# Performance work log

Hardware: AMD Instinct MI355X
Metric: run time of the kernel (lower is better)

## Reference

```python
import jax, jax.numpy as jnp
import numpy as np

N_NODES = 50000
N_EDGES = 800000
N_GRAPHS = 64
EPS = 1e-5
NEG_SLOPE = 0.2


def gat_conv(x, src, dst, W, a_src, a_dst, bias, heads, ch):
    # x: [N, Fin]; W: [Fin, heads*ch]; a_src/a_dst: [heads, ch]; bias: [heads*ch]
    N = x.shape[0]
    h = (x @ W).reshape(N, heads, ch)                       # [N,H,C]
    s_src = jnp.sum(h * a_src, axis=-1)                     # [N,H]
    s_dst = jnp.sum(h * a_dst, axis=-1)                     # [N,H]
    scores = jax.nn.leaky_relu(s_src[src] + s_dst[dst], NEG_SLOPE)  # [E,H]
    m = jax.ops.segment_max(scores, dst, num_segments=N)    # segment softmax (stable)
    e = jnp.exp(scores - m[dst])
    denom = jax.ops.segment_sum(e, dst, num_segments=N)
    alpha = e / denom[dst]                                  # [E,H]
    msg = h[src] * alpha[:, :, None]                        # [E,H,C]
    out = jax.ops.segment_sum(msg, dst, num_segments=N)     # [N,H,C]
    return out.reshape(N, heads * ch) + bias


def batch_norm(x, gamma, beta):
    mu = jnp.mean(x, axis=0)
    var = jnp.var(x, axis=0)  # biased, as in torch BN forward (training mode)
    return gamma * (x - mu) * jax.lax.rsqrt(var + EPS) + beta


def setup_inputs() -> dict:
    key = jax.random.key(0)
    ks = jax.random.split(key, 20)
    x = jax.random.normal(ks[0], (N_NODES, 8), dtype=jnp.float32)
    edge_index = jax.random.randint(ks[1], (2, N_EDGES), 0, N_NODES, dtype=jnp.int32)
    batch = jnp.sort(jax.random.randint(ks[2], (N_NODES,), 0, N_GRAPHS, dtype=jnp.int32))
    g = lambda k, shape: jax.random.normal(k, shape, dtype=jnp.float32) * 0.1
    return {
        "x": x, "edge_index": edge_index, "batch": batch,
        "W1": g(ks[3], (8, 128)), "a_src1": g(ks[4], (4, 32)), "a_dst1": g(ks[5], (4, 32)),
        "b1": jnp.zeros((128,), jnp.float32), "g1": jnp.ones((128,), jnp.float32),
        "beta1": jnp.zeros((128,), jnp.float32),
        "W2": g(ks[6], (128, 256)), "a_src2": g(ks[7], (4, 64)), "a_dst2": g(ks[8], (4, 64)),
        "b2": jnp.zeros((256,), jnp.float32), "g2": jnp.ones((256,), jnp.float32),
        "beta2": jnp.zeros((256,), jnp.float32),
        "fc1_w": g(ks[9], (256, 128)), "fc1_b": jnp.zeros((128,), jnp.float32),
        "fc2_w": g(ks[10], (128, 64)), "fc2_b": jnp.zeros((64,), jnp.float32),
        "fc3_w": g(ks[11], (64, 1)), "fc3_b": jnp.zeros((1,), jnp.float32),
    }


def reference(x, edge_index, batch, W1, a_src1, a_dst1, b1, g1, beta1,
              W2, a_src2, a_dst2, b2, g2, beta2,
              fc1_w, fc1_b, fc2_w, fc2_b, fc3_w, fc3_b):
    N = x.shape[0]
    loop = jnp.arange(N, dtype=edge_index.dtype)
    src = jnp.concatenate([edge_index[0], loop])  # PyG GATConv adds self-loops
    dst = jnp.concatenate([edge_index[1], loop])

    h = gat_conv(x, src, dst, W1, a_src1, a_dst1, b1, heads=4, ch=32)
    h = jax.nn.elu(batch_norm(h, g1, beta1))
    h = gat_conv(h, src, dst, W2, a_src2, a_dst2, b2, heads=4, ch=64)
    h = jax.nn.elu(batch_norm(h, g2, beta2))

    # global mean pool over graphs
    sums = jax.ops.segment_sum(h, batch, num_segments=N_GRAPHS)
    counts = jax.ops.segment_sum(jnp.ones((N,), h.dtype), batch, num_segments=N_GRAPHS)
    pooled = sums / jnp.maximum(counts, 1.0)[:, None]       # [G,256]

    z = jax.nn.relu(pooled @ fc1_w + fc1_b)
    emb = jax.nn.relu(z @ fc2_w + fc2_b)
    out = emb @ fc3_w + fc3_b
    return out.reshape(-1)
```

## Files before the change

### kernel.cpp

```cpp
#include <hip/hip_runtime.h>
#include <hip/hip_bf16.h>
#include <cmath>

#define NSLOPE 0.2f
#define BN_EPS 1e-5f
#define DEGCAP 128

static __device__ __forceinline__ float lrelu(float v) { return v > 0.f ? v : NSLOPE * v; }

static __device__ __forceinline__ float wmax64(float v) {
#pragma unroll
  for (int off = 32; off; off >>= 1) v = fmaxf(v, __shfl_xor(v, off));
  return v;
}
static __device__ __forceinline__ float wsum64(float v) {
#pragma unroll
  for (int off = 32; off; off >>= 1) v += __shfl_xor(v, off);
  return v;
}
static __device__ __forceinline__ float rlf(float v, int j) {
  return __int_as_float(__builtin_amdgcn_readlane(__float_as_int(v), j));
}
static __device__ __forceinline__ unsigned short f2bf(float x) {
  __hip_bfloat16 h = __float2bfloat16(x);
  union { __hip_bfloat16 h; unsigned short u; } c; c.h = h; return c.u;
}
static __device__ __forceinline__ unsigned pack_bf16(float x, float y) {
  return (unsigned)f2bf(x) | ((unsigned)f2bf(y) << 16);
}
static __device__ __forceinline__ float bflo(unsigned p) { return __uint_as_float(p << 16); }
static __device__ __forceinline__ float bfhi(unsigned p) { return __uint_as_float(p & 0xffff0000u); }

__global__ void k_init(int* __restrict__ cnt, int N,
                       const float* __restrict__ W1, const float* __restrict__ as1,
                       const float* __restrict__ ad1, const float* __restrict__ W2,
                       const float* __restrict__ as2, const float* __restrict__ ad2,
                       float* __restrict__ q1s, float* __restrict__ q1d,
                       float* __restrict__ q2s, float* __restrict__ q2d) {
  int i = blockIdx.x * blockDim.x + threadIdx.x;
  int stride = gridDim.x * blockDim.x;
  for (int j = i; j < N; j += stride) cnt[j] = 0;
  if (blockIdx.x == 0) {
    int t = threadIdx.x;
    if (t < 32) {
      int k = t >> 2, h = t & 3;
      float s = 0.f, d = 0.f;
      for (int c = 0; c < 32; ++c) {
        float w = W1[k * 128 + h * 32 + c];
        s = fmaf(w, as1[h * 32 + c], s);
        d = fmaf(w, ad1[h * 32 + c], d);
      }
      q1s[t] = s; q1d[t] = d;
    }
    for (int idx = t; idx < 512; idx += 256) {
      int k = idx >> 2, h = idx & 3;
      float s = 0.f, d = 0.f;
      for (int c = 0; c < 64; ++c) {
        float w = W2[k * 256 + h * 64 + c];
        s = fmaf(w, as2[h * 64 + c], s);
        d = fmaf(w, ad2[h * 64 + c], d);
      }
      q2s[idx] = s; q2d[idx] = d;
    }
  }
}

__global__ void k_scatter(const int* __restrict__ esrc, const int* __restrict__ edst,
                          const int* __restrict__ batch, int E, int N,
                          int* __restrict__ cnt, int* __restrict__ srcs,
                          int* __restrict__ gstart) {
  int i = blockIdx.x * blockDim.x + threadIdx.x;
  int stride = gridDim.x * blockDim.x;
  int total = E + N;
  for (int j = i; j < total; j += stride) {
    int s, d;
    if (j < E) {
      s = esrc[j]; d = edst[j];
    } else {
      int n = j - E;
      s = n; d = n;
      int b = batch[n];
      if (n == 0) {
        for (int g = 0; g <= b; ++g) gstart[g] = 0;
      } else {
        int pb = batch[n - 1];
        if (pb != b)
          for (int g = pb + 1; g <= b; ++g) gstart[g] = n;
      }
      if (n == N - 1)
        for (int g = b + 1; g <= 64; ++g) gstart[g] = N;
    }
    int pos = atomicAdd(&cnt[d], 1);
    if (pos < DEGCAP) srcs[(size_t)d * DEGCAP + pos] = s;
  }
}

__global__ __launch_bounds__(256) void k_s1(const float* __restrict__ x,
                                            const float* __restrict__ q1s,
                                            const float* __restrict__ q1d,
                                            float* __restrict__ ssrc, float* __restrict__ sdst,
                                            int N) {
  __shared__ float qs[32], qd[32];
  int t = threadIdx.x;
  if (t < 32) { qs[t] = q1s[t]; qd[t] = q1d[t]; }
  __syncthreads();
  for (int n = blockIdx.x * 256 + t; n < N; n += gridDim.x * 256) {
    float4 x0 = *(const float4*)&x[n * 8];
    float4 x1 = *(const float4*)&x[n * 8 + 4];
    float xs[8] = {x0.x, x0.y, x0.z, x0.w, x1.x, x1.y, x1.z, x1.w};
    float4 rs = make_float4(0.f, 0.f, 0.f, 0.f);
    float4 rd = make_float4(0.f, 0.f, 0.f, 0.f);
#pragma unroll
    for (int k = 0; k < 8; ++k) {
      rs.x = fmaf(xs[k], qs[k * 4 + 0], rs.x);
      rs.y = fmaf(xs[k], qs[k * 4 + 1], rs.y);
      rs.z = fmaf(xs[k], qs[k * 4 + 2], rs.z);
      rs.w = fmaf(xs[k], qs[k * 4 + 3], rs.w);
      rd.x = fmaf(xs[k], qd[k * 4 + 0], rd.x);
      rd.y = fmaf(xs[k], qd[k * 4 + 1], rd.y);
      rd.z = fmaf(xs[k], qd[k * 4 + 2], rd.z);
      rd.w = fmaf(xs[k], qd[k * 4 + 3], rd.w);
    }
    *(float4*)&ssrc[n * 4] = rs;
    *(float4*)&sdst[n * 4] = rd;
  }
}

__global__ __launch_bounds__(64) void k_agg1(const float* __restrict__ x,
                                             const float* __restrict__ ssrc,
                                             const float* __restrict__ sdst,
                                             const int* __restrict__ cnt,
                                             const int* __restrict__ srcs,
                                             float* __restrict__ agg , int N) {
  int n = blockIdx.x * 64 + threadIdx.x;
  if (n >= N) return;
  int beg = n * DEGCAP;
  int end = beg + min(cnt[n], DEGCAP);
  float4 sd = *(const float4*)&sdst[n * 4];
  float m0 = -INFINITY, m1 = -INFINITY, m2 = -INFINITY, m3 = -INFINITY;
  for (int e = beg; e < end; ++e) {
    int s = srcs[e];
    float4 sv = *(const float4*)&ssrc[s * 4];
    m0 = fmaxf(m0, lrelu(sv.x + sd.x));
    m1 = fmaxf(m1, lrelu(sv.y + sd.y));
    m2 = fmaxf(m2, lrelu(sv.z + sd.z));
    m3 = fmaxf(m3, lrelu(sv.w + sd.w));
  }
  float d0 = 0.f, d1 = 0.f, d2 = 0.f, d3 = 0.f;
  float acc[4][8];
#pragma unroll
  for (int h = 0; h < 4; ++h)
#pragma unroll
    for (int k = 0; k < 8; ++k) acc[h][k] = 0.f;
  const float4* x4 = (const float4*)x;
  for (int e = beg; e < end; ++e) {
    int s = srcs[e];
    float4 sv = *(const float4*)&ssrc[s * 4];
    float w0 = expf(lrelu(sv.x + sd.x) - m0);
    float w1 = expf(lrelu(sv.y + sd.y) - m1);
    float w2 = expf(lrelu(sv.z + sd.z) - m2);
    float w3 = expf(lrelu(sv.w + sd.w) - m3);
    d0 += w0; d1 += w1; d2 += w2; d3 += w3;
    float4 xa = x4[(size_t)s * 2];
    float4 xb = x4[(size_t)s * 2 + 1];
    float xs[8] = {xa.x, xa.y, xa.z, xa.w, xb.x, xb.y, xb.z, xb.w};
    float ws[4] = {w0, w1, w2, w3};
#pragma unroll
    for (int h = 0; h < 4; ++h)
#pragma unroll
      for (int k = 0; k < 8; ++k) acc[h][k] = fmaf(ws[h], xs[k], acc[h][k]);
  }
  float dd[4] = {d0, d1, d2, d3};
#pragma unroll
  for (int h = 0; h < 4; ++h) {
    float inv = 1.0f / dd[h];
    float4 oA = make_float4(acc[h][0] * inv, acc[h][1] * inv, acc[h][2] * inv, acc[h][3] * inv);
    float4 oB = make_float4(acc[h][4] * inv, acc[h][5] * inv, acc[h][6] * inv, acc[h][7] * inv);
    *(float4*)&agg[n * 32 + h * 8] = oA;
    *(float4*)&agg[n * 32 + h * 8 + 4] = oB;
  }
}

__global__ __launch_bounds__(128) void k_stats1(const float* __restrict__ agg,
                                                const float* __restrict__ W1,
                                                const float* __restrict__ b1,
                                                float* __restrict__ part, int N) {
  int t = threadIdx.x;
  __shared__ float ag[32];
  float bb = b1[t];
  float wc[8];
#pragma unroll
  for (int k = 0; k < 8; ++k) wc[k] = W1[k * 128 + t];
  int h = t >> 5;
  float s = 0.f, s2 = 0.f;
  for (int n = blockIdx.x; n < N; n += gridDim.x) {
    if (t < 32) ag[t] = agg[n * 32 + t];
    __syncthreads();
    float v = bb;
#pragma unroll
    for (int k = 0; k < 8; ++k) v = fmaf(ag[h * 8 + k], wc[k], v);
    s += v; s2 += v * v;
    __syncthreads();
  }
  part[(size_t)blockIdx.x * 256 + t] = s;
  part[(size_t)blockIdx.x * 256 + 128 + t] = s2;
}

template <int NB, int TWO_F>
__global__ __launch_bounds__(256) void k_bnreduce2(const float* __restrict__ part,
                                                   float* __restrict__ stat) {
  int j = blockIdx.x, t = threadIdx.x;
  float s = 0.f;
  for (int b = t; b < NB; b += 256) s += part[(size_t)b * TWO_F + j];
#pragma unroll
  for (int off = 32; off; off >>= 1) s += __shfl_xor(s, off);
  __shared__ float red[4];
  if ((t & 63) == 0) red[t >> 6] = s;
  __syncthreads();
  if (t == 0) stat[j] = (red[0] + red[1]) + (red[2] + red[3]);
}

__global__ __launch_bounds__(256) void k_bns2(const float* __restrict__ agg,
                                              const float* __restrict__ W1,
                                              const float* __restrict__ b1,
                                              unsigned* __restrict__ a1h_u,
                                              const float* __restrict__ sum,
                                              const float* __restrict__ sq,
                                              const float* __restrict__ gamma,
                                              const float* __restrict__ beta,
                                              const float* __restrict__ q2s,
                                              const float* __restrict__ q2d,
                                              float* __restrict__ ssrc2,
                                              float* __restrict__ sdst2, int N) {
  int w = threadIdx.x >> 6, l = threadIdx.x & 63;
  int n = blockIdx.x * 4 + w;
  if (n >= N) return;
  int c0 = 2 * l, c1 = 2 * l + 1;
  int h = l >> 4;
  float ag[8];
#pragma unroll
  for (int k = 0; k < 8; ++k) ag[k] = agg[n * 32 + h * 8 + k];
  float v0 = b1[c0], v1 = b1[c1];
#pragma unroll
  for (int k = 0; k < 8; ++k) {
    v0 = fmaf(ag[k], W1[k * 128 + c0], v0);
    v1 = fmaf(ag[k], W1[k * 128 + c1], v1);
  }
  float invN = 1.0f / N;
  float mean0 = sum[c0] * invN, mean1 = sum[c1] * invN;
  float var0 = sq[c0] * invN - mean0 * mean0;
  float var1 = sq[c1] * invN - mean1 * mean1;
  float iv0 = rsqrtf(var0 + BN_EPS), iv1 = rsqrtf(var1 + BN_EPS);
  float y0 = gamma[c0] * ((v0 - mean0) * iv0) + beta[c0];
  float y1 = gamma[c1] * ((v1 - mean1) * iv1) + beta[c1];
  y0 = y0 > 0.f ? y0 : expm1f(y0);
  y1 = y1 > 0.f ? y1 : expm1f(y1);
  a1h_u[(size_t)n * 64 + l] = pack_bf16(y0, y1);
  float4 qs0 = *(const float4*)&q2s[c0 * 4];
  float4 qs1 = *(const float4*)&q2s[c1 * 4];
  float4 qd0 = *(const float4*)&q2d[c0 * 4];
  float4 qd1 = *(const float4*)&q2d[c1 * 4];
  float p0 = fmaf(y1, qs1.x, y0 * qs0.x);
  float p1 = fmaf(y1, qs1.y, y0 * qs0.y);
  float p2 = fmaf(y1, qs1.z, y0 * qs0.z);
  float p3 = fmaf(y1, qs1.w, y0 * qs0.w);
  float d0 = fmaf(y1, qd1.x, y0 * qd0.x);
  float d1 = fmaf(y1, qd1.y, y0 * qd0.y);
  float d2 = fmaf(y1, qd1.z, y0 * qd0.z);
  float d3 = fmaf(y1, qd1.w, y0 * qd0.w);
#pragma unroll
  for (int off = 32; off; off >>= 1) {
    p0 += __shfl_xor(p0, off); p1 += __shfl_xor(p1, off);
    p2 += __shfl_xor(p2, off); p3 += __shfl_xor(p3, off);
    d0 += __shfl_xor(d0, off); d1 += __shfl_xor(d1, off);
    d2 += __shfl_xor(d2, off); d3 += __shfl_xor(d3, off);
  }
  if (l == 0) {
    *(float4*)&ssrc2[n * 4] = make_float4(p0, p1, p2, p3);
    *(float4*)&sdst2[n * 4] = make_float4(d0, d1, d2, d3);
  }
}

__global__ __launch_bounds__(256) void k_agg2(const unsigned short* __restrict__ a1h,
                                              const float* __restrict__ ssrc,
                                              const float* __restrict__ sdst,
                                              const int* __restrict__ cnt,
                                              const int* __restrict__ srcs,
                                              unsigned* __restrict__ aggh , int N) {
  int wid = threadIdx.x >> 6, l = threadIdx.x & 63;
  int n = blockIdx.x * 4 + wid;
  if (n >= N) return;
  int beg = n * DEGCAP;
  int deg = min(cnt[n], DEGCAP);
  float4 sd = *(const float4*)&sdst[n * 4];
  float m0 = -INFINITY, m1 = -INFINITY, m2 = -INFINITY, m3 = -INFINITY;
  float d0 = 0.f, d1 = 0.f, d2 = 0.f, d3 = 0.f;
  float2 ac0 = {0.f, 0.f}, ac1 = {0.f, 0.f}, ac2 = {0.f, 0.f}, ac3 = {0.f, 0.f};
  for (int c0 = 0; c0 < deg; c0 += 64) {
    int e = c0 + l;
    bool act = e < deg;
    int s = act ? srcs[beg + e] : 0;
    float4 sv = *(const float4*)&ssrc[s * 4];
    float v0 = act ? lrelu(sv.x + sd.x) : -INFINITY;
    float v1 = act ? lrelu(sv.y + sd.y) : -INFINITY;
    float v2 = act ? lrelu(sv.z + sd.z) : -INFINITY;
    float v3 = act ? lrelu(sv.w + sd.w) : -INFINITY;
    float nm0 = fmaxf(m0, wmax64(v0)), nm1 = fmaxf(m1, wmax64(v1));
    float nm2 = fmaxf(m2, wmax64(v2)), nm3 = fmaxf(m3, wmax64(v3));
    float sc0 = expf(m0 - nm0), sc1 = expf(m1 - nm1);
    float sc2 = expf(m2 - nm2), sc3 = expf(m3 - nm3);
    m0 = nm0; m1 = nm1; m2 = nm2; m3 = nm3;
    float ev0 = act ? expf(v0 - m0) : 0.f;
    float ev1 = act ? expf(v1 - m1) : 0.f;
    float ev2 = act ? expf(v2 - m2) : 0.f;
    float ev3 = act ? expf(v3 - m3) : 0.f;
    d0 = d0 * sc0 + wsum64(ev0);
    d1 = d1 * sc1 + wsum64(ev1);
    d2 = d2 * sc2 + wsum64(ev2);
    d3 = d3 * sc3 + wsum64(ev3);
    ac0.x *= sc0; ac0.y *= sc0; ac1.x *= sc1; ac1.y *= sc1;
    ac2.x *= sc2; ac2.y *= sc2; ac3.x *= sc3; ac3.y *= sc3;
    int cn = min(64, deg - c0);
    int cn4 = (cn + 3) & ~3;
    for (int j = 0; j < cn4; j += 4) {
      int sA = __builtin_amdgcn_readlane(s, j);
      int sB = __builtin_amdgcn_readlane(s, j + 1);
      int sC = __builtin_amdgcn_readlane(s, j + 2);
      int sD = __builtin_amdgcn_readlane(s, j + 3);
      unsigned pA = *(const unsigned*)&a1h[(size_t)sA * 128 + 2 * l];
      unsigned pB = *(const unsigned*)&a1h[(size_t)sB * 128 + 2 * l];
      unsigned pC = *(const unsigned*)&a1h[(size_t)sC * 128 + 2 * l];
      unsigned pD = *(const unsigned*)&a1h[(size_t)sD * 128 + 2 * l];
      float wA0 = rlf(ev0, j),     wA1 = rlf(ev1, j),     wA2 = rlf(ev2, j),     wA3 = rlf(ev3, j);
      float wB0 = rlf(ev0, j + 1), wB1 = rlf(ev1, j + 1), wB2 = rlf(ev2, j + 1), wB3 = rlf(ev3, j + 1);
      float wC0 = rlf(ev0, j + 2), wC1 = rlf(ev1, j + 2), wC2 = rlf(ev2, j + 2), wC3 = rlf(ev3, j + 2);
      float wD0 = rlf(ev0, j + 3), wD1 = rlf(ev1, j + 3), wD2 = rlf(ev2, j + 3), wD3 = rlf(ev3, j + 3);
      float ax, ay;
      ax = bflo(pA); ay = bfhi(pA);
      ac0.x = fmaf(wA0, ax, ac0.x); ac0.y = fmaf(wA0, ay, ac0.y);
      ac1.x = fmaf(wA1, ax, ac1.x); ac1.y = fmaf(wA1, ay, ac1.y);
      ac2.x = fmaf(wA2, ax, ac2.x); ac2.y = fmaf(wA2, ay, ac2.y);
      ac3.x = fmaf(wA3, ax, ac3.x); ac3.y = fmaf(wA3, ay, ac3.y);
      ax = bflo(pB); ay = bfhi(pB);
      ac0.x = fmaf(wB0, ax, ac0.x); ac0.y = fmaf(wB0, ay, ac0.y);
      ac1.x = fmaf(wB1, ax, ac1.x); ac1.y = fmaf(wB1, ay, ac1.y);
      ac2.x = fmaf(wB2, ax, ac2.x); ac2.y = fmaf(wB2, ay, ac2.y);
      ac3.x = fmaf(wB3, ax, ac3.x); ac3.y = fmaf(wB3, ay, ac3.y);
      ax = bflo(pC); ay = bfhi(pC);
      ac0.x = fmaf(wC0, ax, ac0.x); ac0.y = fmaf(wC0, ay, ac0.y);
      ac1.x = fmaf(wC1, ax, ac1.x); ac1.y = fmaf(wC1, ay, ac1.y);
      ac2.x = fmaf(wC2, ax, ac2.x); ac2.y = fmaf(wC2, ay, ac2.y);
      ac3.x = fmaf(wC3, ax, ac3.x); ac3.y = fmaf(wC3, ay, ac3.y);
      ax = bflo(pD); ay = bfhi(pD);
      ac0.x = fmaf(wD0, ax, ac0.x); ac0.y = fmaf(wD0, ay, ac0.y);
      ac1.x = fmaf(wD1, ax, ac1.x); ac1.y = fmaf(wD1, ay, ac1.y);
      ac2.x = fmaf(wD2, ax, ac2.x); ac2.y = fmaf(wD2, ay, ac2.y);
      ac3.x = fmaf(wD3, ax, ac3.x); ac3.y = fmaf(wD3, ay, ac3.y);
    }
  }
  size_t pl = (size_t)N * 64;
  size_t base = (size_t)n * 64 + l;
  float i0 = 1.0f / d0, i1 = 1.0f / d1, i2 = 1.0f / d2, i3 = 1.0f / d3;
  aggh[base] = pack_bf16(ac0.x * i0, ac0.y * i0);
  aggh[pl + base] = pack_bf16(ac1.x * i1, ac1.y * i1);
  aggh[2 * pl + base] = pack_bf16(ac2.x * i2, ac2.y * i2);
  aggh[3 * pl + base] = pack_bf16(ac3.x * i3, ac3.y * i3);
}

__global__ __launch_bounds__(256) void k_post2(const unsigned short* __restrict__ aggh,
                                               const float* __restrict__ W2,
                                               const float* __restrict__ b2,
                                               unsigned* __restrict__ o2h,
                                               float* __restrict__ part, int N) {
  __shared__ float As[64][64];
  __shared__ float Bs[64][64];
  int h = blockIdx.y;
  int m0 = blockIdx.x * 64;
  int tid = threadIdx.x;
  const unsigned short* Ap = aggh + (size_t)h * N * 128;
  int tx = tid & 15, ty = tid >> 4;
  float acc[4][4];
#pragma unroll
  for (int r = 0; r < 4; ++r)
#pragma unroll
    for (int c = 0; c < 4; ++c) acc[r][c] = 0.f;

#pragma unroll
  for (int kc = 0; kc < 2; ++kc) {
    {
      int ml = tid & 63, kg = tid >> 6;
      const unsigned short* arow = Ap + (size_t)(m0 + ml) * 128 + kc * 64 + kg * 16;
      bool rok = (m0 + ml) < N;
#pragma unroll
      for (int it = 0; it < 2; ++it) {
        uint4 q = rok ? *(const uint4*)(arow + it * 8) : make_uint4(0, 0, 0, 0);
        int kb = kg * 16 + it * 8;
        As[kb + 0][ml] = bflo(q.x); As[kb + 1][ml] = bfhi(q.x);
        As[kb + 2][ml] = bflo(q.y); As[kb + 3][ml] = bfhi(q.y);
        As[kb + 4][ml] = bflo(q.z); As[kb + 5][ml] = bfhi(q.z);
        As[kb + 6][ml] = bflo(q.w); As[kb + 7][ml] = bfhi(q.w);
      }
    }
    {
      int c4 = tid & 15, k0 = tid >> 4;
      for (int k = k0; k < 64; k += 16) {
        float4 v = *(const float4*)&W2[(size_t)(kc * 64 + k) * 256 + h * 64 + c4 * 4];
        *(float4*)&Bs[k][c4 * 4] = v;
      }
    }
    __syncthreads();
#pragma unroll 2
    for (int k = 0; k < 64; ++k) {
      float4 a4 = *(const float4*)&As[k][ty * 4];
      float4 b4 = *(const float4*)&Bs[k][tx * 4];
      float av[4] = {a4.x, a4.y, a4.z, a4.w};
      float bv[4] = {b4.x, b4.y, b4.z, b4.w};
#pragma unroll
      for (int r = 0; r < 4; ++r)
#pragma unroll
        for (int c = 0; c < 4; ++c) acc[r][c] = fmaf(av[r], bv[c], acc[r][c]);
    }
    __syncthreads();
  }

  float4 bb = *(const float4*)&b2[h * 64 + tx * 4];
  float ps[4] = {0.f, 0.f, 0.f, 0.f};
  float pq[4] = {0.f, 0.f, 0.f, 0.f};
#pragma unroll
  for (int r = 0; r < 4; ++r) {
    int row = m0 + ty * 4 + r;
    if (row < N) {
      float4 c4;
      c4.x = acc[r][0] + bb.x; c4.y = acc[r][1] + bb.y;
      c4.z = acc[r][2] + bb.z; c4.w = acc[r][3] + bb.w;
      uint2 pw;
      pw.x = pack_bf16(c4.x, c4.y);
      pw.y = pack_bf16(c4.z, c4.w);
      *(uint2*)&o2h[(size_t)row * 128 + (h * 64 + tx * 4) / 2] = pw;
      ps[0] += c4.x; pq[0] += c4.x * c4.x;
      ps[1] += c4.y; pq[1] += c4.y * c4.y;
      ps[2] += c4.z; pq[2] += c4.z * c4.z;
      ps[3] += c4.w; pq[3] += c4.w * c4.w;
    }
  }
  __syncthreads();
  float* red = &As[0][0];
#pragma unroll
  for (int c = 0; c < 4; ++c) {
    red[ty * 64 + tx * 4 + c] = ps[c];
    red[1024 + ty * 64 + tx * 4 + c] = pq[c];
  }
  __syncthreads();
  if (tid < 128) {
    int isq = tid >> 6, col = tid & 63;
    float s = 0.f;
#pragma unroll
    for (int w = 0; w < 16; ++w) s += red[isq * 1024 + w * 64 + col];
    part[((size_t)blockIdx.x * 4 + h) * 128 + isq * 64 + col] = s;
  }
}

__global__ __launch_bounds__(256) void k_bnredpost(const float* __restrict__ part, int nmb,
                                                   float* __restrict__ stat) {
  int j = blockIdx.x;
  int isq = j >> 8, col = j & 255;
  int h = col >> 6, cw = col & 63;
  int t = threadIdx.x;
  float s = 0.f;
  for (int mb = t; mb < nmb; mb += 256) s += part[((size_t)mb * 4 + h) * 128 + isq * 64 + cw];
#pragma unroll
  for (int off = 32; off; off >>= 1) s += __shfl_xor(s, off);
  __shared__ float red[4];
  if ((t & 63) == 0) red[t >> 6] = s;
  __syncthreads();
  if (t == 0) stat[j] = (red[0] + red[1]) + (red[2] + red[3]);
}

__global__ __launch_bounds__(256) void k_poolbn(const unsigned* __restrict__ o2h,
                                                const int* __restrict__ gstart,
                                                const float* __restrict__ sum,
                                                const float* __restrict__ sq,
                                                const float* __restrict__ gamma,
                                                const float* __restrict__ beta,
                                                float* __restrict__ part, int N) {
  int g = blockIdx.x, by = blockIdx.y, t = threadIdx.x;
  float mean = sum[t] * (1.0f / N);
  float var = sq[t] * (1.0f / N) - mean * mean;
  float inv = rsqrtf(var + BN_EPS);
  float ga = gamma[t], be = beta[t];
  int r0 = gstart[g], r1 = gstart[g + 1];
  int u = t >> 1, hi = t & 1;
  float s = 0.f;
  for (int base = r0 + by * 128; base < r1; base += 16 * 128) {
    int lim = min(r1, base + 128);
    for (int r = base; r < lim; ++r) {
      unsigned pw = o2h[(size_t)r * 128 + u];
      float v = hi ? bfhi(pw) : bflo(pw);
      float y = ga * ((v - mean) * inv) + be;
      s += (y > 0.f ? y : expm1f(y));
    }
  }
  part[((size_t)g * 16 + by) * 256 + t] = s;
}

__global__ __launch_bounds__(256) void k_head(const float* __restrict__ poolpart,
                                              const int* __restrict__ gstart,
                                              const float* __restrict__ w1, const float* __restrict__ b1,
                                              const float* __restrict__ w2, const float* __restrict__ b2,
                                              const float* __restrict__ w3, const float* __restrict__ b3,
                                              float* __restrict__ out) {
  __shared__ float p[256], z1[128], z2[64];
  int g = blockIdx.x, t = threadIdx.x;
  float s0 = 0.f;
#pragma unroll
  for (int b = 0; b < 16; ++b) s0 += poolpart[((size_t)g * 16 + b) * 256 + t];
  float cnt = (float)(gstart[g + 1] - gstart[g]);
  p[t] = s0 / fmaxf(cnt, 1.0f);
  __syncthreads();
  if (t < 128) {
    float s = b1[t];
    for (int k = 0; k < 256; ++k) s = fmaf(p[k], w1[k * 128 + t], s);
    z1[t] = fmaxf(s, 0.f);
  }
  __syncthreads();
  if (t < 64) {
    float s = b2[t];
    for (int k = 0; k < 128; ++k) s = fmaf(z1[k], w2[k * 64 + t], s);
    z2[t] = fmaxf(s, 0.f);
  }
  __syncthreads();
  if (t < 64) {
    float s = z2[t] * w3[t];
#pragma unroll
    for (int off = 32; off; off >>= 1) s += __shfl_xor(s, off);
    if (t == 0) out[g] = s + b3[0];
  }
}

extern "C" void kernel_launch(void* const* d_in, const int* in_sizes, int n_in,
                              void* d_out, int out_size, void* d_ws, size_t ws_size,
                              hipStream_t stream) {
  const float* x    = (const float*)d_in[0];
  const int*   eidx = (const int*)d_in[1];
  const int*   batch= (const int*)d_in[2];
  const float* W1   = (const float*)d_in[3];
  const float* as1  = (const float*)d_in[4];
  const float* ad1  = (const float*)d_in[5];
  const float* b1   = (const float*)d_in[6];
  const float* g1   = (const float*)d_in[7];
  const float* be1  = (const float*)d_in[8];
  const float* W2   = (const float*)d_in[9];
  const float* as2  = (const float*)d_in[10];
  const float* ad2  = (const float*)d_in[11];
  const float* b2   = (const float*)d_in[12];
  const float* g2   = (const float*)d_in[13];
  const float* be2  = (const float*)d_in[14];
  const float* fc1w = (const float*)d_in[15];
  const float* fc1b = (const float*)d_in[16];
  const float* fc2w = (const float*)d_in[17];
  const float* fc2b = (const float*)d_in[18];
  const float* fc3w = (const float*)d_in[19];
  const float* fc3b = (const float*)d_in[20];
  float* out = (float*)d_out;
  (void)n_in; (void)out_size; (void)ws_size;

  int N = in_sizes[0] / 8;
  int E = in_sizes[1] / 2;
  const int* esrc = eidx;
  const int* edst = eidx + E;
  int nmb = (N + 63) / 64;

  char* w = (char*)d_ws;
  auto take = [&](size_t bytes) -> char* {
    char* r = w;
    w += (bytes + 255) & ~(size_t)255;
    return r;
  };
  int*   cnt     = (int*)take(4 * (size_t)N);
  int*   srcs    = (int*)take(4 * (size_t)N * DEGCAP);
  int*   gstart  = (int*)take(4 * 65);
  float* bnstat  = (float*)take(4 * 1024);
  float* bnpart  = (float*)take(4 * 524288);
  float* pp2     = (float*)take(4 * (size_t)nmb * 512);
  float* poolpart= (float*)take(4 * 64 * 16 * 256);
  float* q1s     = (float*)take(4 * 32);
  float* q1d     = (float*)take(4 * 32);
  float* q2s     = (float*)take(4 * 512);
  float* q2d     = (float*)take(4 * 512);
  float* ssrc1   = (float*)take(16 * (size_t)N);
  float* sdst1   = (float*)take(16 * (size_t)N);
  float* ssrc2   = (float*)take(16 * (size_t)N);
  float* sdst2   = (float*)take(16 * (size_t)N);
  float* agg1    = (float*)take(4 * (size_t)N * 32);
  unsigned short* a1h  = (unsigned short*)take(2 * (size_t)N * 128);
  unsigned short* aggh = (unsigned short*)take(2 * (size_t)N * 512);
  unsigned* o2h  = (unsigned*)take(4 * (size_t)N * 128);

  float* sum1 = bnstat;       float* sq1 = bnstat + 128;
  float* sum2 = bnstat + 256; float* sq2 = bnstat + 512;

  k_init<<<196, 256, 0, stream>>>(cnt, N, W1, as1, ad1, W2, as2, ad2, q1s, q1d, q2s, q2d);
  k_scatter<<<2048, 256, 0, stream>>>(esrc, edst, batch, E, N, cnt, srcs, gstart);

  k_s1<<<256, 256, 0, stream>>>(x, q1s, q1d, ssrc1, sdst1, N);
  k_agg1<<<(N + 63) / 64, 64, 0, stream>>>(x, ssrc1, sdst1, cnt, srcs, agg1, N);
  k_stats1<<<2048, 128, 0, stream>>>(agg1, W1, b1, bnpart, N);
  k_bnreduce2<2048, 256><<<256, 256, 0, stream>>>(bnpart, bnstat);
  k_bns2<<<(N + 3) / 4, 256, 0, stream>>>(agg1, W1, b1, (unsigned*)a1h, sum1, sq1, g1, be1,
                                          q2s, q2d, ssrc2, sdst2, N);

  k_agg2<<<(N + 3) / 4, 256, 0, stream>>>(a1h, ssrc2, sdst2, cnt, srcs, (unsigned*)aggh, N);
  k_post2<<<dim3(nmb, 4), 256, 0, stream>>>(aggh, W2, b2, o2h, pp2, N);
  k_bnredpost<<<512, 256, 0, stream>>>(pp2, nmb, sum2);

  k_poolbn<<<dim3(64, 16), 256, 0, stream>>>(o2h, gstart, sum2, sq2, g2, be2, poolpart, N);
  k_head<<<64, 256, 0, stream>>>(poolpart, gstart, fc1w, fc1b, fc2w, fc2b, fc3w, fc3b, out);
}
```

Before: 335.3 us.

## Split agg1 per head, stage agg2 weights in LDS, merge init into scatter

k_agg1 now uses four threads per node, one per head, instead of one thread per node. This spreads the gather and FMA work across more lanes and cuts per-thread register use. k_agg2 writes the per-chunk softmax weights and source indices to shared memory and reads them back as vectors, replacing many readlane instructions. The separate init kernel is replaced by a memset, and the attention-vector precompute is folded into the scatter kernel, removing one launch. Risks are redundant loads of x in agg1 (four threads read the same row) and an LDS write/read hazard in agg2 with no explicit barrier, though it is wave-local.

```diff
diff --git a/kernel.cpp b/kernel.cpp
--- a/kernel.cpp
+++ b/kernel.cpp
@@ -18,9 +18,6 @@
   for (int off = 32; off; off >>= 1) v += __shfl_xor(v, off);
   return v;
 }
-static __device__ __forceinline__ float rlf(float v, int j) {
-  return __int_as_float(__builtin_amdgcn_readlane(__float_as_int(v), j));
-}
 static __device__ __forceinline__ unsigned short f2bf(float x) {
   __hip_bfloat16 h = __float2bfloat16(x);
   union { __hip_bfloat16 h; unsigned short u; } c; c.h = h; return c.u;
@@ -31,15 +28,15 @@
 static __device__ __forceinline__ float bflo(unsigned p) { return __uint_as_float(p << 16); }
 static __device__ __forceinline__ float bfhi(unsigned p) { return __uint_as_float(p & 0xffff0000u); }
 
-__global__ void k_init(int* __restrict__ cnt, int N,
-                       const float* __restrict__ W1, const float* __restrict__ as1,
-                       const float* __restrict__ ad1, const float* __restrict__ W2,
-                       const float* __restrict__ as2, const float* __restrict__ ad2,
-                       float* __restrict__ q1s, float* __restrict__ q1d,
-                       float* __restrict__ q2s, float* __restrict__ q2d) {
-  int i = blockIdx.x * blockDim.x + threadIdx.x;
-  int stride = gridDim.x * blockDim.x;
-  for (int j = i; j < N; j += stride) cnt[j] = 0;
+__global__ void k_scatter(const int* __restrict__ esrc, const int* __restrict__ edst,
+                          const int* __restrict__ batch, int E, int N,
+                          int* __restrict__ cnt, int* __restrict__ srcs,
+                          int* __restrict__ gstart,
+                          const float* __restrict__ W1, const float* __restrict__ as1,
+                          const float* __restrict__ ad1, const float* __restrict__ W2,
+                          const float* __restrict__ as2, const float* __restrict__ ad2,
+                          float* __restrict__ q1s, float* __restrict__ q1d,
+                          float* __restrict__ q2s, float* __restrict__ q2d) {
   if (blockIdx.x == 0) {
     int t = threadIdx.x;
     if (t < 32) {
@@ -63,12 +60,6 @@
       q2s[idx] = s; q2d[idx] = d;
     }
   }
-}
-
-__global__ void k_scatter(const int* __restrict__ esrc, const int* __restrict__ edst,
-                          const int* __restrict__ batch, int E, int N,
-                          int* __restrict__ cnt, int* __restrict__ srcs,
-                          int* __restrict__ gstart) {
   int i = blockIdx.x * blockDim.x + threadIdx.x;
   int stride = gridDim.x * blockDim.x;
   int total = E + N;
@@ -126,59 +117,44 @@
   }
 }
 
-__global__ __launch_bounds__(64) void k_agg1(const float* __restrict__ x,
-                                             const float* __restrict__ ssrc,
-                                             const float* __restrict__ sdst,
-                                             const int* __restrict__ cnt,
-                                             const int* __restrict__ srcs,
-                                             float* __restrict__ agg , int N) {
-  int n = blockIdx.x * 64 + threadIdx.x;
+__global__ __launch_bounds__(256) void k_agg1(const float* __restrict__ x,
+                                              const float* __restrict__ ssrc,
+                                              const float* __restrict__ sdst,
+                                              const int* __restrict__ cnt,
+                                              const int* __restrict__ srcs,
+                                              float* __restrict__ agg , int N) {
+  int tid = blockIdx.x * 256 + threadIdx.x;
+  int n = tid >> 2, h = tid & 3;
   if (n >= N) return;
   int beg = n * DEGCAP;
   int end = beg + min(cnt[n], DEGCAP);
-  float4 sd = *(const float4*)&sdst[n * 4];
-  float m0 = -INFINITY, m1 = -INFINITY, m2 = -INFINITY, m3 = -INFINITY;
+  float sd = sdst[n * 4 + h];
+  float m = -INFINITY;
   for (int e = beg; e < end; ++e) {
     int s = srcs[e];
-    float4 sv = *(const float4*)&ssrc[s * 4];
-    m0 = fmaxf(m0, lrelu(sv.x + sd.x));
-    m1 = fmaxf(m1, lrelu(sv.y + sd.y));
-    m2 = fmaxf(m2, lrelu(sv.z + sd.z));
-    m3 = fmaxf(m3, lrelu(sv.w + sd.w));
-  }
-  float d0 = 0.f, d1 = 0.f, d2 = 0.f, d3 = 0.f;
-  float acc[4][8];
-#pragma unroll
-  for (int h = 0; h < 4; ++h)
-#pragma unroll
-    for (int k = 0; k < 8; ++k) acc[h][k] = 0.f;
+    m = fmaxf(m, lrelu(ssrc[s * 4 + h] + sd));
+  }
+  float d = 0.f;
+  float acc[8];
+#pragma unroll
+  for (int k = 0; k < 8; ++k) acc[k] = 0.f;
   const float4* x4 = (const float4*)x;
   for (int e = beg; e < end; ++e) {
     int s = srcs[e];
-    float4 sv = *(const float4*)&ssrc[s * 4];
-    float w0 = expf(lrelu(sv.x + sd.x) - m0);
-    float w1 = expf(lrelu(sv.y + sd.y) - m1);
-    float w2 = expf(lrelu(sv.z + sd.z) - m2);
-    float w3 = expf(lrelu(sv.w + sd.w) - m3);
-    d0 += w0; d1 += w1; d2 += w2; d3 += w3;
+    float w = expf(lrelu(ssrc[s * 4 + h] + sd) - m);
+    d += w;
     float4 xa = x4[(size_t)s * 2];
     float4 xb = x4[(size_t)s * 2 + 1];
-    float xs[8] = {xa.x, xa.y, xa.z, xa.w, xb.x, xb.y, xb.z, xb.w};
-    float ws[4] = {w0, w1, w2, w3};
-#pragma unroll
-    for (int h = 0; h < 4; ++h)
-#pragma unroll
-      for (int k = 0; k < 8; ++k) acc[h][k] = fmaf(ws[h], xs[k], acc[h][k]);
-  }
-  float dd[4] = {d0, d1, d2, d3};
-#pragma unroll
-  for (int h = 0; h < 4; ++h) {
-    float inv = 1.0f / dd[h];
-    float4 oA = make_float4(acc[h][0] * inv, acc[h][1] * inv, acc[h][2] * inv, acc[h][3] * inv);
-    float4 oB = make_float4(acc[h][4] * inv, acc[h][5] * inv, acc[h][6] * inv, acc[h][7] * inv);
-    *(float4*)&agg[n * 32 + h * 8] = oA;
-    *(float4*)&agg[n * 32 + h * 8 + 4] = oB;
-  }
+    acc[0] = fmaf(w, xa.x, acc[0]); acc[1] = fmaf(w, xa.y, acc[1]);
+    acc[2] = fmaf(w, xa.z, acc[2]); acc[3] = fmaf(w, xa.w, acc[3]);
+    acc[4] = fmaf(w, xb.x, acc[4]); acc[5] = fmaf(w, xb.y, acc[5]);
+    acc[6] = fmaf(w, xb.z, acc[6]); acc[7] = fmaf(w, xb.w, acc[7]);
+  }
+  float inv = 1.0f / d;
+  float4 oA = make_float4(acc[0] * inv, acc[1] * inv, acc[2] * inv, acc[3] * inv);
+  float4 oB = make_float4(acc[4] * inv, acc[5] * inv, acc[6] * inv, acc[7] * inv);
+  *(float4*)&agg[n * 32 + h * 8] = oA;
+  *(float4*)&agg[n * 32 + h * 8 + 4] = oB;
 }
 
 __global__ __launch_bounds__(128) void k_stats1(const float* __restrict__ agg,
@@ -281,12 +257,14 @@
   }
 }
 
-__global__ __launch_bounds__(256) void k_agg2(const unsigned short* __restrict__ a1h,
+__global__ __launch_bounds__(256) void k_agg2(const unsigned* __restrict__ a1h_u,
                                               const float* __restrict__ ssrc,
                                               const float* __restrict__ sdst,
                                               const int* __restrict__ cnt,
                                               const int* __restrict__ srcs,
                                               unsigned* __restrict__ aggh , int N) {
+  __shared__ float evl[4][64][4];
+  __shared__ int sil[4][64];
   int wid = threadIdx.x >> 6, l = threadIdx.x & 63;
   int n = blockIdx.x * 4 + wid;
   if (n >= N) return;
@@ -320,42 +298,41 @@
     d3 = d3 * sc3 + wsum64(ev3);
     ac0.x *= sc0; ac0.y *= sc0; ac1.x *= sc1; ac1.y *= sc1;
     ac2.x *= sc2; ac2.y *= sc2; ac3.x *= sc3; ac3.y *= sc3;
+    *(float4*)&evl[wid][l][0] = make_float4(ev0, ev1, ev2, ev3);
+    sil[wid][l] = s;
     int cn = min(64, deg - c0);
     int cn4 = (cn + 3) & ~3;
     for (int j = 0; j < cn4; j += 4) {
-      int sA = __builtin_amdgcn_readlane(s, j);
-      int sB = __builtin_amdgcn_readlane(s, j + 1);
-      int sC = __builtin_amdgcn_readlane(s, j + 2);
-      int sD = __builtin_amdgcn_readlane(s, j + 3);
-      unsigned pA = *(const unsigned*)&a1h[(size_t)sA * 128 + 2 * l];
-      unsigned pB = *(const unsigned*)&a1h[(size_t)sB * 128 + 2 * l];
-      unsigned pC = *(const unsigned*)&a1h[(size_t)sC * 128 + 2 * l];
-      unsigned pD = *(const unsigned*)&a1h[(size_t)sD * 128 + 2 * l];
-      float wA0 = rlf(ev0, j),     wA1 = rlf(ev1, j),     wA2 = rlf(ev2, j),     wA3 = rlf(ev3, j);
-      float wB0 = rlf(ev0, j + 1), wB1 = rlf(ev1, j + 1), wB2 = rlf(ev2, j + 1), wB3 = rlf(ev3, j + 1);
-      float wC0 = rlf(ev0, j + 2), wC1 = rlf(ev1, j + 2), wC2 = rlf(ev2, j + 2), wC3 = rlf(ev3, j + 2);
-      float wD0 = rlf(ev0, j + 3), wD1 = rlf(ev1, j + 3), wD2 = rlf(ev2, j + 3), wD3 = rlf(ev3, j + 3);
+      int4 s4 = *(const int4*)&sil[wid][j];
+      float4 wA = *(const float4*)&evl[wid][j][0];
+      float4 wB = *(const float4*)&evl[wid][j + 1][0];
+      float4 wC = *(const float4*)&evl[wid][j + 2][0];
+      float4 wD = *(const float4*)&evl[wid][j + 3][0];
+      unsigned pA = a1h_u[(size_t)s4.x * 64 + l];
+      unsigned pB = a1h_u[(size_t)s4.y * 64 + l];
+      unsigned pC = a1h_u[(size_t)s4.z * 64 + l];
+      unsigned pD = a1h_u[(size_t)s4.w * 64 + l];
       float ax, ay;
       ax = bflo(pA); ay = bfhi(pA);
-      ac0.x = fmaf(wA0, ax, ac0.x); ac0.y = fmaf(wA0, ay, ac0.y);
-      ac1.x = fmaf(wA1, ax, ac1.x); ac1.y = fmaf(wA1, ay, ac1.y);
-      ac2.x = fmaf(wA2, ax, ac2.x); ac2.y = fmaf(wA2, ay, ac2.y);
-      ac3.x = fmaf(wA3, ax, ac3.x); ac3.y = fmaf(wA3, ay, ac3.y);
+      ac0.x = fmaf(wA.x, ax, ac0.x); ac0.y = fmaf(wA.x, ay, ac0.y);
+      ac1.x = fmaf(wA.y, ax, ac1.x); ac1.y = fmaf(wA.y, ay, ac1.y);
+      ac2.x = fmaf(wA.z, ax, ac2.x); ac2.y = fmaf(wA.z, ay, ac2.y);
+      ac3.x = fmaf(wA.w, ax, ac3.x); ac3.y = fmaf(wA.w, ay, ac3.y);
       ax = bflo(pB); ay = bfhi(pB);
-      ac0.x = fmaf(wB0, ax, ac0.x); ac0.y = fmaf(wB0, ay, ac0.y);
-      ac1.x = fmaf(wB1, ax, ac1.x); ac1.y = fmaf(wB1, ay, ac1.y);
-      ac2.x = fmaf(wB2, ax, ac2.x); ac2.y = fmaf(wB2, ay, ac2.y);
-      ac3.x = fmaf(wB3, ax, ac3.x); ac3.y = fmaf(wB3, ay, ac3.y);
+      ac0.x = fmaf(wB.x, ax, ac0.x); ac0.y = fmaf(wB.x, ay, ac0.y);
+      ac1.x = fmaf(wB.y, ax, ac1.x); ac1.y = fmaf(wB.y, ay, ac1.y);
+      ac2.x = fmaf(wB.z, ax, ac2.x); ac2.y = fmaf(wB.z, ay, ac2.y);
+      ac3.x = fmaf(wB.w, ax, ac3.x); ac3.y = fmaf(wB.w, ay, ac3.y);
       ax = bflo(pC); ay = bfhi(pC);
-      ac0.x = fmaf(wC0, ax, ac0.x); ac0.y = fmaf(wC0, ay, ac0.y);
-      ac1.x = fmaf(wC1, ax, ac1.x); ac1.y = fmaf(wC1, ay, ac1.y);
-      ac2.x = fmaf(wC2, ax, ac2.x); ac2.y = fmaf(wC2, ay, ac2.y);
-      ac3.x = fmaf(wC3, ax, ac3.x); ac3.y = fmaf(wC3, ay, ac3.y);
+      ac0.x = fmaf(wC.x, ax, ac0.x); ac0.y = fmaf(wC.x, ay, ac0.y);
+      ac1.x = fmaf(wC.y, ax, ac1.x); ac1.y = fmaf(wC.y, ay, ac1.y);
+      ac2.x = fmaf(wC.z, ax, ac2.x); ac2.y = fmaf(wC.z, ay, ac2.y);
+      ac3.x = fmaf(wC.w, ax, ac3.x); ac3.y = fmaf(wC.w, ay, ac3.y);
       ax = bflo(pD); ay = bfhi(pD);
-      ac0.x = fmaf(wD0, ax, ac0.x); ac0.y = fmaf(wD0, ay, ac0.y);
-      ac1.x = fmaf(wD1, ax, ac1.x); ac1.y = fmaf(wD1, ay, ac1.y);
-      ac2.x = fmaf(wD2, ax, ac2.x); ac2.y = fmaf(wD2, ay, ac2.y);
-      ac3.x = fmaf(wD3, ax, ac3.x); ac3.y = fmaf(wD3, ay, ac3.y);
+      ac0.x = fmaf(wD.x, ax, ac0.x); ac0.y = fmaf(wD.x, ay, ac0.y);
+      ac1.x = fmaf(wD.y, ax, ac1.x); ac1.y = fmaf(wD.y, ay, ac1.y);
+      ac2.x = fmaf(wD.z, ax, ac2.x); ac2.y = fmaf(wD.z, ay, ac2.y);
+      ac3.x = fmaf(wD.w, ax, ac3.x); ac3.y = fmaf(wD.w, ay, ac3.y);
     }
   }
   size_t pl = (size_t)N * 64;
@@ -599,17 +576,19 @@
   float* sum1 = bnstat;       float* sq1 = bnstat + 128;
   float* sum2 = bnstat + 256; float* sq2 = bnstat + 512;
 
-  k_init<<<196, 256, 0, stream>>>(cnt, N, W1, as1, ad1, W2, as2, ad2, q1s, q1d, q2s, q2d);
-  k_scatter<<<2048, 256, 0, stream>>>(esrc, edst, batch, E, N, cnt, srcs, gstart);
+  hipMemsetAsync(cnt, 0, 4 * (size_t)N, stream);
+  k_scatter<<<2048, 256, 0, stream>>>(esrc, edst, batch, E, N, cnt, srcs, gstart,
+                                      W1, as1, ad1, W2, as2, ad2, q1s, q1d, q2s, q2d);
 
   k_s1<<<256, 256, 0, stream>>>(x, q1s, q1d, ssrc1, sdst1, N);
-  k_agg1<<<(N + 63) / 64, 64, 0, stream>>>(x, ssrc1, sdst1, cnt, srcs, agg1, N);
+  k_agg1<<<(4 * N + 255) / 256, 256, 0, stream>>>(x, ssrc1, sdst1, cnt, srcs, agg1, N);
   k_stats1<<<2048, 128, 0, stream>>>(agg1, W1, b1, bnpart, N);
   k_bnreduce2<2048, 256><<<256, 256, 0, stream>>>(bnpart, bnstat);
   k_bns2<<<(N + 3) / 4, 256, 0, stream>>>(agg1, W1, b1, (unsigned*)a1h, sum1, sq1, g1, be1,
                                           q2s, q2d, ssrc2, sdst2, N);
 
-  k_agg2<<<(N + 3) / 4, 256, 0, stream>>>(a1h, ssrc2, sdst2, cnt, srcs, (unsigned*)aggh, N);
+  k_agg2<<<(N + 3) / 4, 256, 0, stream>>>((const unsigned*)a1h, ssrc2, sdst2, cnt, srcs,
+                                          (unsigned*)aggh, N);
   k_post2<<<dim3(nmb, 4), 256, 0, stream>>>(aggh, W2, b2, o2h, pp2, N);
   k_bnredpost<<<512, 256, 0, stream>>>(pp2, nmb, sum2);
 
```

New measurement: 326.1 us. 2.7% less time.
